# Performance work log

Hardware: AMD Instinct MI355X
Metric: run time of the kernel (lower is better)

## Reference

```python
import jax, jax.numpy as jnp
import numpy as np

# Hardcoded hyperparameters from the torch module
E = 128   # n_embd
H = 4     # n_head
HS = 32   # head_size = n_embd // n_head
L = 4     # n_layer
T = 512   # block_size (full context)
V = 512   # vocab_size (quantization_levels)
B = 64    # batch
SCALE = 0.02  # init std per _init_weights


def _ln(x, g, b):
    mu = x.mean(-1, keepdims=True)
    var = ((x - mu) ** 2).mean(-1, keepdims=True)
    return (x - mu) / jnp.sqrt(var + 1e-5) * g + b


def setup_inputs() -> dict:
    key = jax.random.key(0)
    ks = jax.random.split(key, 24)
    rn = lambda k, shape: SCALE * jax.random.normal(k, shape, dtype=jnp.float32)
    return {
        "idx": jax.random.randint(ks[0], (B, T), 0, V),
        "tok_emb": rn(ks[1], (V, E)),
        "pos_emb": rn(ks[2], (T, E)),
        # per-head projections, stacked over layers and heads: x[...,E] @ wq[l,h] -> [...,HS]
        "wq": rn(ks[3], (L, H, E, HS)),
        "wk": rn(ks[4], (L, H, E, HS)),
        "wv": rn(ks[5], (L, H, E, HS)),
        "w_proj": rn(ks[6], (L, E, E)),   # torch Linear weight layout [out, in]
        "b_proj": jnp.zeros((L, E), jnp.float32),
        "ln1_g": jnp.ones((L, E), jnp.float32),
        "ln1_b": jnp.zeros((L, E), jnp.float32),
        "ln2_g": jnp.ones((L, E), jnp.float32),
        "ln2_b": jnp.zeros((L, E), jnp.float32),
        "w1": rn(ks[7], (L, 4 * E, E)),
        "b1": jnp.zeros((L, 4 * E), jnp.float32),
        "w2": rn(ks[8], (L, E, 4 * E)),
        "b2": jnp.zeros((L, E), jnp.float32),
        "lnf_g": jnp.ones((E,), jnp.float32),
        "lnf_b": jnp.zeros((E,), jnp.float32),
        "w_head": rn(ks[9], (V, E)),
        "b_head": jnp.zeros((V,), jnp.float32),
    }


def reference(idx, tok_emb, pos_emb, wq, wk, wv, w_proj, b_proj,
              ln1_g, ln1_b, ln2_g, ln2_b, w1, b1, w2, b2,
              lnf_g, lnf_b, w_head, b_head):
    Bv, Tv = idx.shape
    x = tok_emb[idx] + pos_emb[None, :Tv, :]          # [B,T,E]
    causal = jnp.tril(jnp.ones((Tv, Tv), dtype=bool))
    for l in range(L):
        h = _ln(x, ln1_g[l], ln1_b[l])
        q = jnp.einsum('bte,hed->bhtd', h, wq[l])     # [B,H,T,HS]
        k = jnp.einsum('bte,hed->bhtd', h, wk[l])
        v = jnp.einsum('bte,hed->bhtd', h, wv[l])
        s = jnp.einsum('bhtd,bhsd->bhts', q, k) * (HS ** -0.5)
        s = jnp.where(causal, s, -jnp.inf)
        a = jax.nn.softmax(s, axis=-1)
        o = jnp.einsum('bhts,bhsd->bhtd', a, v)       # [B,H,T,HS]
        o = o.transpose(0, 2, 1, 3).reshape(Bv, Tv, E)  # concat heads
        x = x + o @ w_proj[l].T + b_proj[l]
        h = _ln(x, ln2_g[l], ln2_b[l])
        x = x + jax.nn.gelu(h @ w1[l].T + b1[l], approximate=False) @ w2[l].T + b2[l]
    x = _ln(x, lnf_g, lnf_b)
    logits = x @ w_head.T + b_head                    # [B,T,V]
    return logits
```

## Files before the change

kernel.cpp:

```cpp
#include <hip/hip_runtime.h>

typedef __bf16 bf16x8 __attribute__((ext_vector_type(8)));
typedef __bf16 bf16x2 __attribute__((ext_vector_type(2)));
typedef float f32x4 __attribute__((ext_vector_type(4)));

constexpr int E_ = 128, H_ = 4, HS_ = 32, L_ = 4, T_ = 512, V_ = 512, B_ = 64;
constexpr int M_ = B_ * T_;

__device__ __forceinline__ float b2f(ushort u) {
    return __uint_as_float(((uint)u) << 16);
}
__device__ __forceinline__ ushort f2b(float f) {
    uint x = __float_as_uint(f);
    uint r = (x + 0x7fffu + ((x >> 16) & 1u)) >> 16;
    return (ushort)r;
}
__device__ __forceinline__ uint packbf(float a, float b) {
    bf16x2 t; t[0] = (__bf16)a; t[1] = (__bf16)b;
    return __builtin_bit_cast(uint, t);
}

constexpr int kNSeg = 19;
constexpr int kOffs[kNSeg + 1] = {
    0, 65536, 131072, 196608, 262144, 327680, 393216, 393728, 394240, 394752,
    395264, 395776, 657920, 659968, 922112, 922624, 922752, 922880, 988416, 988928
};
constexpr int kTotal = 988928;

struct SrcPtrs { const void* p[kNSeg]; };

__global__ __launch_bounds__(256) void k_convert(SrcPtrs sp, ushort* __restrict__ arena) {
    int gid = blockIdx.x * 256 + threadIdx.x;
    if (gid >= kTotal) return;
    bool isf32 = (((const uint*)sp.p[7])[0] == 0x3F800000u);
    int s = 0;
    #pragma unroll
    for (int i = 1; i < kNSeg; i++) if (gid >= kOffs[i]) s = i;
    int local = gid - kOffs[s];
    ushort v;
    if (isf32) v = f2b(((const float*)sp.p[s])[local]);
    else       v = ((const ushort*)sp.p[s])[local];
    arena[gid] = v;
}

__global__ void k_prep_qkv(const ushort* __restrict__ wq, const ushort* __restrict__ wk,
                           const ushort* __restrict__ wv, ushort* __restrict__ wt) {
    int gid = blockIdx.x * 256 + threadIdx.x;
    if (gid >= L_ * 384 * E_) return;
    int e = gid & 127;
    int n = (gid >> 7) % 384;
    int l = gid / (384 * E_);
    int part = n >> 7, within = n & 127, hh = within >> 5, d = within & 31;
    const ushort* src = part == 0 ? wq : (part == 1 ? wk : wv);
    wt[gid] = src[(((size_t)(l * H_ + hh) * E_) + e) * HS_ + d];
}

__global__ __launch_bounds__(256) void k_embed_ln(const int* __restrict__ idx,
                                                  const ushort* __restrict__ tok,
                                                  const ushort* __restrict__ pos,
                                                  const ushort* __restrict__ g,
                                                  const ushort* __restrict__ beta,
                                                  float* __restrict__ x, ushort* __restrict__ h) {
    int wave = threadIdx.x >> 6, lane = threadIdx.x & 63;
    int row = blockIdx.x * 4 + wave;
    int t = row & (T_ - 1);
    int id = idx[row];
    float v0 = b2f(tok[id * E_ + lane])      + b2f(pos[t * E_ + lane]);
    float v1 = b2f(tok[id * E_ + lane + 64]) + b2f(pos[t * E_ + lane + 64]);
    size_t o = (size_t)row * E_;
    x[o + lane] = v0; x[o + lane + 64] = v1;
    float s = v0 + v1;
    #pragma unroll
    for (int m = 32; m; m >>= 1) s += __shfl_xor(s, m, 64);
    float mu = s * (1.0f / 128.0f);
    float d0 = v0 - mu, d1 = v1 - mu;
    float ss = d0 * d0 + d1 * d1;
    #pragma unroll
    for (int m = 32; m; m >>= 1) ss += __shfl_xor(ss, m, 64);
    float rstd = rsqrtf(ss * (1.0f / 128.0f) + 1e-5f);
    h[o + lane]      = f2b(d0 * rstd * b2f(g[lane])      + b2f(beta[lane]));
    h[o + lane + 64] = f2b(d1 * rstd * b2f(g[lane + 64]) + b2f(beta[lane + 64]));
}

template<int EPI>
__global__ __launch_bounds__(256) void k_gemm(const ushort* __restrict__ A, const ushort* __restrict__ W,
                                              const ushort* __restrict__ bias, void* __restrict__ outp,
                                              void* __restrict__ outp2,
                                              const ushort* __restrict__ lng, const ushort* __restrict__ lnb,
                                              const uint* __restrict__ dtraw, int K, int lda, int ldc) {
    int wid = threadIdx.x >> 6, lane = threadIdx.x & 63;
    int wr = wid >> 1, wc = wid & 1;
    int bm = blockIdx.x, bn = blockIdx.y;
    int r16 = lane & 15, kq = lane >> 4;
    const ushort* Abase = A + (size_t)(bm * 128 + wr * 64 + r16) * lda + kq * 8;
    const ushort* Wbase = W + (size_t)(bn * 128 + wc * 64 + r16) * K + kq * 8;
    bool f32out = false;
    if constexpr (EPI == 1) f32out = (dtraw[0] == 0x3F800000u);
    f32x4 acc[4][4];
    #pragma unroll
    for (int i = 0; i < 4; i++)
        #pragma unroll
        for (int j = 0; j < 4; j++) acc[i][j] = (f32x4)0.0f;
    for (int k0 = 0; k0 < K; k0 += 32) {
        bf16x8 af[4], wf[4];
        #pragma unroll
        for (int mi = 0; mi < 4; mi++)
            af[mi] = *(const bf16x8*)(Abase + (size_t)mi * 16 * lda + k0);
        #pragma unroll
        for (int ni = 0; ni < 4; ni++)
            wf[ni] = *(const bf16x8*)(Wbase + (size_t)ni * 16 * K + k0);
        #pragma unroll
        for (int mi = 0; mi < 4; mi++)
            #pragma unroll
            for (int ni = 0; ni < 4; ni++)
                acc[mi][ni] = __builtin_amdgcn_mfma_f32_16x16x32_bf16(af[mi], wf[ni], acc[mi][ni], 0, 0, 0);
    }
    int orow0 = bm * 128 + wr * 64 + kq * 4;
    int ocol0 = bn * 128 + wc * 64 + r16;
    if constexpr (EPI == 5) {
        __shared__ float lnS[2][128], lnQ[2][128];
        float*  xg = (float*)outp;
        ushort* hg = (ushort*)outp2;
        #pragma unroll
        for (int ni = 0; ni < 4; ni++) {
            int col = ocol0 + ni * 16;
            float bv = b2f(bias[col]);
            #pragma unroll
            for (int mi = 0; mi < 4; mi++) {
                #pragma unroll
                for (int e = 0; e < 4; e++) {
                    size_t gi = (size_t)(orow0 + mi * 16 + e) * 128 + col;
                    float xv = xg[gi] + acc[mi][ni][e] + bv;
                    xg[gi] = xv;
                    acc[mi][ni][e] = xv;
                }
            }
        }
        #pragma unroll
        for (int mi = 0; mi < 4; mi++) {
            #pragma unroll
            for (int e = 0; e < 4; e++) {
                float s = 0.f, q = 0.f;
                #pragma unroll
                for (int ni = 0; ni < 4; ni++) { float v = acc[mi][ni][e]; s += v; q += v * v; }
                #pragma unroll
                for (int mk = 1; mk < 16; mk <<= 1) {
                    s += __shfl_xor(s, mk, 64); q += __shfl_xor(q, mk, 64);
                }
                if (r16 == 0) {
                    int lrow = wr * 64 + mi * 16 + kq * 4 + e;
                    lnS[wc][lrow] = s; lnQ[wc][lrow] = q;
                }
            }
        }
        __syncthreads();
        float gc[4], bc[4];
        #pragma unroll
        for (int ni = 0; ni < 4; ni++) {
            int col = ocol0 + ni * 16;
            gc[ni] = b2f(lng[col]); bc[ni] = b2f(lnb[col]);
        }
        #pragma unroll
        for (int mi = 0; mi < 4; mi++) {
            #pragma unroll
            for (int e = 0; e < 4; e++) {
                int lrow = wr * 64 + mi * 16 + kq * 4 + e;
                float tot = lnS[0][lrow] + lnS[1][lrow];
                float tq  = lnQ[0][lrow] + lnQ[1][lrow];
                float mu  = tot * (1.0f / 128.0f);
                float var = tq * (1.0f / 128.0f) - mu * mu;
                float rstd = rsqrtf(var + 1e-5f);
                size_t grow = (size_t)(bm * 128 + lrow) * 128;
                #pragma unroll
                for (int ni = 0; ni < 4; ni++) {
                    int col = ocol0 + ni * 16;
                    hg[grow + col] = f2b((acc[mi][ni][e] - mu) * rstd * gc[ni] + bc[ni]);
                }
            }
        }
        return;
    }
    if constexpr (EPI == 4) {
        if (bn == 2) {
            ushort* vt = (ushort*)outp2;
            #pragma unroll
            for (int mi = 0; mi < 4; mi++) {
                int row0 = orow0 + mi * 16;
                int bb = row0 >> 9, tt = row0 & 511;
                #pragma unroll
                for (int ni = 0; ni < 4; ni++) {
                    int vd = (ocol0 - 256) + ni * 16;
                    int hh = vd >> 5, dd = vd & 31;
                    ushort4 pk;
                    pk.x = f2b(acc[mi][ni][0]); pk.y = f2b(acc[mi][ni][1]);
                    pk.z = f2b(acc[mi][ni][2]); pk.w = f2b(acc[mi][ni][3]);
                    *(ushort4*)(vt + (((size_t)(bb * 4 + hh) * 32 + dd) << 9) + tt) = pk;
                }
            }
            return;
        }
    }
    #pragma unroll
    for (int mi = 0; mi < 4; mi++) {
        #pragma unroll
        for (int ni = 0; ni < 4; ni++) {
            int col = ocol0 + ni * 16;
            float bv = 0.0f;
            if constexpr (EPI == 1 || EPI == 2) bv = b2f(bias[col]);
            #pragma unroll
            for (int e = 0; e < 4; e++) {
                int row = orow0 + mi * 16 + e;
                float v = acc[mi][ni][e] + bv;
                if constexpr (EPI == 2) v = 0.5f * v * (1.0f + erff(v * 0.70710678118f));
                if constexpr (EPI == 1) {
                    if (f32out) ((float*)outp)[(size_t)row * ldc + col] = v;
                    else        ((ushort*)outp)[(size_t)row * ldc + col] = f2b(v);
                } else {
                    ((ushort*)outp)[(size_t)row * ldc + col] = f2b(v);
                }
            }
        }
    }
}

constexpr float SC_ = 0.2550348637f;

__device__ __forceinline__ bf16x8 scale8(bf16x8 v, float s) {
    bf16x8 r;
    #pragma unroll
    for (int i = 0; i < 8; i++) r[i] = (__bf16)((float)v[i] * s);
    return r;
}

__device__ __forceinline__ bf16x8 relayoutP(const float* p, int r16, int g) {
    uint pk00 = packbf(p[0], p[1]), pk01 = packbf(p[2], p[3]);
    uint pk10 = packbf(p[4], p[5]), pk11 = packbf(p[6], p[7]);
    int ga = ((g & 1) << 5) + r16;
    int gb = ga + 16;
    uint A0 = (uint)__shfl((int)pk00, ga), A1 = (uint)__shfl((int)pk01, ga);
    uint C0 = (uint)__shfl((int)pk00, gb), C1 = (uint)__shfl((int)pk01, gb);
    uint B0 = (uint)__shfl((int)pk10, ga), B1 = (uint)__shfl((int)pk11, ga);
    uint D0 = (uint)__shfl((int)pk10, gb), D1 = (uint)__shfl((int)pk11, gb);
    bool hi2 = g >= 2;
    uint4 pr;
    pr.x = hi2 ? B0 : A0; pr.y = hi2 ? B1 : A1;
    pr.z = hi2 ? D0 : C0; pr.w = hi2 ? D1 : C1;
    return __builtin_bit_cast(bf16x8, pr);
}

__global__ __launch_bounds__(256) void k_attn_proj(const ushort* __restrict__ qk,
                                                   const ushort* __restrict__ vt,
                                                   const ushort* __restrict__ wproj,
                                                   const ushort* __restrict__ bproj,
                                                   const ushort* __restrict__ lng,
                                                   const ushort* __restrict__ lnb,
                                                   float* __restrict__ x,
                                                   ushort* __restrict__ h) {
    __shared__ ushort olds[32 * 128];
    __shared__ float lnS[4][32], lnQ[4][32];
    int lane = threadIdx.x & 63, w = threadIdx.x >> 6;
    int r16 = lane & 15, g = lane >> 4;
    int bid = blockIdx.x;
    int b = (bid & 7) * 8 + (bid >> 7);
    int p = (bid >> 3) & 15;
    int qbaseA = p * 16, qbaseB = (31 - p) * 16;
    int myqA = qbaseA + r16, myqB = qbaseB + r16;
    int qmaxA = qbaseA + 15, qmaxB = qbaseB + 15;
    const ushort* qkbase = qk + (size_t)b * 512 * 256;
    bf16x8 qfA = scale8(*(const bf16x8*)(qkbase + (size_t)(qbaseA + r16) * 256 + w * 32 + g * 8), SC_);
    bf16x8 qfB = scale8(*(const bf16x8*)(qkbase + (size_t)(qbaseB + r16) * 256 + w * 32 + g * 8), SC_);
    const ushort* kptr = qkbase + 128 + w * 32 + g * 8;
    const ushort* vbase = vt + ((size_t)(b * 4 + w) * 32) * 512;

    f32x4 oA0 = (f32x4)0.0f, oA1 = (f32x4)0.0f, oB0 = (f32x4)0.0f, oB1 = (f32x4)0.0f;
    float psA = 0.0f, psB = 0.0f;
    for (int j0 = 0; j0 <= qmaxB; j0 += 32) {
        bf16x8 kf0 = *(const bf16x8*)(kptr + (size_t)(j0 + r16) * 256);
        bf16x8 kf1 = *(const bf16x8*)(kptr + (size_t)(j0 + 16 + r16) * 256);
        bf16x8 vf0 = *(const bf16x8*)(vbase + (size_t)r16 * 512 + j0 + g * 8);
        bf16x8 vf1 = *(const bf16x8*)(vbase + (size_t)(16 + r16) * 512 + j0 + g * 8);
        {
            f32x4 s0 = __builtin_amdgcn_mfma_f32_16x16x32_bf16(kf0, qfB, (f32x4)0.0f, 0, 0, 0);
            f32x4 s1 = __builtin_amdgcn_mfma_f32_16x16x32_bf16(kf1, qfB, (f32x4)0.0f, 0, 0, 0);
            float pv[8];
            #pragma unroll
            for (int e = 0; e < 4; e++) {
                int ja = j0 + 4 * g + e;
                pv[e]     = (ja      <= myqB) ? exp2f(s0[e]) : 0.0f;
                pv[4 + e] = (ja + 16 <= myqB) ? exp2f(s1[e]) : 0.0f;
                psB += pv[e] + pv[4 + e];
            }
            bf16x8 pf = relayoutP(pv, r16, g);
            oB0 = __builtin_amdgcn_mfma_f32_16x16x32_bf16(vf0, pf, oB0, 0, 0, 0);
            oB1 = __builtin_amdgcn_mfma_f32_16x16x32_bf16(vf1, pf, oB1, 0, 0, 0);
        }
        if (j0 <= qmaxA) {
            f32x4 s0 = __builtin_amdgcn_mfma_f32_16x16x32_bf16(kf0, qfA, (f32x4)0.0f, 0, 0, 0);
            f32x4 s1 = __builtin_amdgcn_mfma_f32_16x16x32_bf16(kf1, qfA, (f32x4)0.0f, 0, 0, 0);
            float pv[8];
            #pragma unroll
            for (int e = 0; e < 4; e++) {
                int ja = j0 + 4 * g + e;
                pv[e]     = (ja      <= myqA) ? exp2f(s0[e]) : 0.0f;
                pv[4 + e] = (ja + 16 <= myqA) ? exp2f(s1[e]) : 0.0f;
                psA += pv[e] + pv[4 + e];
            }
            bf16x8 pf = relayoutP(pv, r16, g);
            oA0 = __builtin_amdgcn_mfma_f32_16x16x32_bf16(vf0, pf, oA0, 0, 0, 0);
            oA1 = __builtin_amdgcn_mfma_f32_16x16x32_bf16(vf1, pf, oA1, 0, 0, 0);
        }
    }
    psA += __shfl_xor(psA, 16, 64); psA += __shfl_xor(psA, 32, 64);
    psB += __shfl_xor(psB, 16, 64); psB += __shfl_xor(psB, 32, 64);
    {
        float invA = 1.0f / psA, invB = 1.0f / psB;
        int sw = (r16 & 7) << 4;
        int baseA = r16 * 256 + w * 64 + g * 8;
        int baseB = (16 + r16) * 256 + w * 64 + g * 8;
        uint2 a0, a1, b0, b1;
        a0.x = packbf(oA0[0] * invA, oA0[1] * invA); a0.y = packbf(oA0[2] * invA, oA0[3] * invA);
        a1.x = packbf(oA1[0] * invA, oA1[1] * invA); a1.y = packbf(oA1[2] * invA, oA1[3] * invA);
        b0.x = packbf(oB0[0] * invB, oB0[1] * invB); b0.y = packbf(oB0[2] * invB, oB0[3] * invB);
        b1.x = packbf(oB1[0] * invB, oB1[1] * invB); b1.y = packbf(oB1[2] * invB, oB1[3] * invB);
        *(uint2*)((char*)olds + (baseA ^ sw))        = a0;
        *(uint2*)((char*)olds + ((baseA + 32) ^ sw)) = a1;
        *(uint2*)((char*)olds + (baseB ^ sw))        = b0;
        *(uint2*)((char*)olds + ((baseB + 32) ^ sw)) = b1;
    }
    __syncthreads();
    f32x4 acc[2][2];
    acc[0][0] = (f32x4)0.0f; acc[0][1] = (f32x4)0.0f;
    acc[1][0] = (f32x4)0.0f; acc[1][1] = (f32x4)0.0f;
    const ushort* wp0 = wproj + (size_t)(w * 32 + r16) * 128 + g * 8;
    const ushort* wp1 = wp0 + (size_t)16 * 128;
    #pragma unroll
    for (int kk = 0; kk < 4; kk++) {
        bf16x8 w0 = *(const bf16x8*)(wp0 + kk * 32);
        bf16x8 w1 = *(const bf16x8*)(wp1 + kk * 32);
        #pragma unroll
        for (int mi = 0; mi < 2; mi++) {
            int abyte = ((mi * 16 + r16) * 256 + kk * 64 + g * 16) ^ ((r16 & 7) << 4);
            bf16x8 af = *(const bf16x8*)((const char*)olds + abyte);
            acc[mi][0] = __builtin_amdgcn_mfma_f32_16x16x32_bf16(af, w0, acc[mi][0], 0, 0, 0);
            acc[mi][1] = __builtin_amdgcn_mfma_f32_16x16x32_bf16(af, w1, acc[mi][1], 0, 0, 0);
        }
    }
    int col0 = w * 32 + r16, col1 = col0 + 16;
    float bv0 = b2f(bproj[col0]), bv1 = b2f(bproj[col1]);
    float xv[2][2][4];
    #pragma unroll
    for (int mi = 0; mi < 2; mi++) {
        int qb = mi == 0 ? qbaseA : qbaseB;
        #pragma unroll
        for (int e = 0; e < 4; e++) {
            size_t gi = (size_t)(b * 512 + qb + g * 4 + e) * 128;
            float v0 = x[gi + col0] + acc[mi][0][e] + bv0;
            float v1 = x[gi + col1] + acc[mi][1][e] + bv1;
            x[gi + col0] = v0; x[gi + col1] = v1;
            xv[mi][0][e] = v0; xv[mi][1][e] = v1;
        }
    }
    #pragma unroll
    for (int mi = 0; mi < 2; mi++) {
        #pragma unroll
        for (int e = 0; e < 4; e++) {
            float s = xv[mi][0][e] + xv[mi][1][e];
            float q = xv[mi][0][e] * xv[mi][0][e] + xv[mi][1][e] * xv[mi][1][e];
            #pragma unroll
            for (int mk = 1; mk < 16; mk <<= 1) {
                s += __shfl_xor(s, mk, 64); q += __shfl_xor(q, mk, 64);
            }
            if (r16 == 0) { lnS[w][mi * 16 + g * 4 + e] = s; lnQ[w][mi * 16 + g * 4 + e] = q; }
        }
    }
    __syncthreads();
    float g0 = b2f(lng[col0]), g1 = b2f(lng[col1]);
    float be0 = b2f(lnb[col0]), be1 = b2f(lnb[col1]);
    #pragma unroll
    for (int mi = 0; mi < 2; mi++) {
        int qb = mi == 0 ? qbaseA : qbaseB;
        #pragma unroll
        for (int e = 0; e < 4; e++) {
            int lr = mi * 16 + g * 4 + e;
            float tot = lnS[0][lr] + lnS[1][lr] + lnS[2][lr] + lnS[3][lr];
            float tq  = lnQ[0][lr] + lnQ[1][lr] + lnQ[2][lr] + lnQ[3][lr];
            float mu  = tot * (1.0f / 128.0f);
            float var = tq * (1.0f / 128.0f) - mu * mu;
            float rstd = rsqrtf(var + 1e-5f);
            size_t gr = (size_t)(b * 512 + qb + g * 4 + e) * 128;
            h[gr + col0] = f2b((xv[mi][0][e] - mu) * rstd * g0 + be0);
            h[gr + col1] = f2b((xv[mi][1][e] - mu) * rstd * g1 + be1);
        }
    }
}

extern "C" void kernel_launch(void* const* d_in, const int* in_sizes, int n_in,
                              void* d_out, int out_size, void* d_ws, size_t ws_size,
                              hipStream_t stream) {
    const int* idx = (const int*)d_in[0];

    char* ws = (char*)d_ws;
    float*  x     = (float*) (ws + 0);
    ushort* h     = (ushort*)(ws + (16u << 20));
    ushort* wqkvt = (ushort*)(ws + (24u << 20));
    ushort* arena = (ushort*)(ws + (25u << 20));

    ushort* qkv = (ushort*)d_out;
    ushort* vt  = (ushort*)d_out + (12u << 20);
    ushort* mid = (ushort*)d_out;

    const ushort* tok    = arena + kOffs[0];
    const ushort* pos    = arena + kOffs[1];
    const ushort* wqp    = arena + kOffs[2];
    const ushort* wkp    = arena + kOffs[3];
    const ushort* wvp    = arena + kOffs[4];
    const ushort* w_proj = arena + kOffs[5];
    const ushort* b_proj = arena + kOffs[6];
    const ushort* ln1_g  = arena + kOffs[7];
    const ushort* ln1_b  = arena + kOffs[8];
    const ushort* ln2_g  = arena + kOffs[9];
    const ushort* ln2_b  = arena + kOffs[10];
    const ushort* w1     = arena + kOffs[11];
    const ushort* b1     = arena + kOffs[12];
    const ushort* w2     = arena + kOffs[13];
    const ushort* b2     = arena + kOffs[14];
    const ushort* lnf_g  = arena + kOffs[15];
    const ushort* lnf_b  = arena + kOffs[16];
    const ushort* w_head = arena + kOffs[17];
    const ushort* b_head = arena + kOffs[18];

    SrcPtrs sp;
    for (int i = 0; i < kNSeg; i++) sp.p[i] = d_in[i + 1];
    k_convert<<<(kTotal + 255) / 256, 256, 0, stream>>>(sp, arena);

    k_prep_qkv<<<768, 256, 0, stream>>>(wqp, wkp, wvp, wqkvt);
    k_embed_ln<<<M_ / 4, 256, 0, stream>>>(idx, tok, pos, ln1_g, ln1_b, x, h);
    for (int l = 0; l < L_; l++) {
        const ushort* ng = (l < 3) ? (ln1_g + (l + 1) * E_) : lnf_g;
        const ushort* nb = (l < 3) ? (ln1_b + (l + 1) * E_) : lnf_b;
        k_gemm<4><<<dim3(M_ / 128, 3), 256, 0, stream>>>(h, wqkvt + (size_t)l * 384 * E_, nullptr,
                                                         qkv, vt, nullptr, nullptr, nullptr, 128, 128, 256);
        k_attn_proj<<<1024, 256, 0, stream>>>(qkv, vt, w_proj + (size_t)l * E_ * E_, b_proj + l * E_,
                                              ln2_g + l * E_, ln2_b + l * E_, x, h);
        k_gemm<2><<<dim3(M_ / 128, 4), 256, 0, stream>>>(h, w1 + (size_t)l * 4 * E_ * E_, b1 + l * 4 * E_,
                                                         mid, nullptr, nullptr, nullptr, nullptr, 128, 128, 512);
        k_gemm<5><<<dim3(M_ / 128, 1), 256, 0, stream>>>(mid, w2 + (size_t)l * E_ * 4 * E_, b2 + l * E_,
                                                         x, h, ng, nb, nullptr, 512, 512, 128);
    }
    k_gemm<1><<<dim3(M_ / 128, 4), 256, 0, stream>>>(h, w_head, b_head, d_out, nullptr,
                                                     nullptr, nullptr, (const uint*)d_in[8], 128, 128, 512);
}
```

Baseline: 500.3 us.

## Fuse MLP up/down GEMMs into one kernel with LDS-resident hidden activations

Replaces the separate W1+GELU GEMM and the W2+residual+LayerNorm GEMM with a single kernel. Each 64-row block computes the 512-wide hidden layer in four 128-column chunks, keeps each GELU'd chunk in swizzled LDS, and accumulates the down projection in registers. This avoids writing and re-reading the large bf16 intermediate in global memory and removes one launch per layer. The attention loop also gains register double-buffering of K/V loads. The cost is extra syncthreads per chunk and more register pressure.

Result: faster. 457.2 us (-8.6%).

```diff
diff --git a/kernel.cpp b/kernel.cpp
--- a/kernel.cpp
+++ b/kernel.cpp
@@ -86,7 +86,6 @@
 __global__ __launch_bounds__(256) void k_gemm(const ushort* __restrict__ A, const ushort* __restrict__ W,
                                               const ushort* __restrict__ bias, void* __restrict__ outp,
                                               void* __restrict__ outp2,
-                                              const ushort* __restrict__ lng, const ushort* __restrict__ lnb,
                                               const uint* __restrict__ dtraw, int K, int lda, int ldc) {
     int wid = threadIdx.x >> 6, lane = threadIdx.x & 63;
     int wr = wid >> 1, wc = wid & 1;
@@ -117,69 +116,6 @@
     }
     int orow0 = bm * 128 + wr * 64 + kq * 4;
     int ocol0 = bn * 128 + wc * 64 + r16;
-    if constexpr (EPI == 5) {
-        __shared__ float lnS[2][128], lnQ[2][128];
-        float*  xg = (float*)outp;
-        ushort* hg = (ushort*)outp2;
-        #pragma unroll
-        for (int ni = 0; ni < 4; ni++) {
-            int col = ocol0 + ni * 16;
-            float bv = b2f(bias[col]);
-            #pragma unroll
-            for (int mi = 0; mi < 4; mi++) {
-                #pragma unroll
-                for (int e = 0; e < 4; e++) {
-                    size_t gi = (size_t)(orow0 + mi * 16 + e) * 128 + col;
-                    float xv = xg[gi] + acc[mi][ni][e] + bv;
-                    xg[gi] = xv;
-                    acc[mi][ni][e] = xv;
-                }
-            }
-        }
-        #pragma unroll
-        for (int mi = 0; mi < 4; mi++) {
-            #pragma unroll
-            for (int e = 0; e < 4; e++) {
-                float s = 0.f, q = 0.f;
-                #pragma unroll
-                for (int ni = 0; ni < 4; ni++) { float v = acc[mi][ni][e]; s += v; q += v * v; }
-                #pragma unroll
-                for (int mk = 1; mk < 16; mk <<= 1) {
-                    s += __shfl_xor(s, mk, 64); q += __shfl_xor(q, mk, 64);
-                }
-                if (r16 == 0) {
-                    int lrow = wr * 64 + mi * 16 + kq * 4 + e;
-                    lnS[wc][lrow] = s; lnQ[wc][lrow] = q;
-                }
-            }
-        }
-        __syncthreads();
-        float gc[4], bc[4];
-        #pragma unroll
-        for (int ni = 0; ni < 4; ni++) {
-            int col = ocol0 + ni * 16;
-            gc[ni] = b2f(lng[col]); bc[ni] = b2f(lnb[col]);
-        }
-        #pragma unroll
-        for (int mi = 0; mi < 4; mi++) {
-            #pragma unroll
-            for (int e = 0; e < 4; e++) {
-                int lrow = wr * 64 + mi * 16 + kq * 4 + e;
-                float tot = lnS[0][lrow] + lnS[1][lrow];
-                float tq  = lnQ[0][lrow] + lnQ[1][lrow];
-                float mu  = tot * (1.0f / 128.0f);
-                float var = tq * (1.0f / 128.0f) - mu * mu;
-                float rstd = rsqrtf(var + 1e-5f);
-                size_t grow = (size_t)(bm * 128 + lrow) * 128;
-                #pragma unroll
-                for (int ni = 0; ni < 4; ni++) {
-                    int col = ocol0 + ni * 16;
-                    hg[grow + col] = f2b((acc[mi][ni][e] - mu) * rstd * gc[ni] + bc[ni]);
-                }
-            }
-        }
-        return;
-    }
     if constexpr (EPI == 4) {
         if (bn == 2) {
             ushort* vt = (ushort*)outp2;
@@ -206,12 +142,11 @@
         for (int ni = 0; ni < 4; ni++) {
             int col = ocol0 + ni * 16;
             float bv = 0.0f;
-            if constexpr (EPI == 1 || EPI == 2) bv = b2f(bias[col]);
+            if constexpr (EPI == 1) bv = b2f(bias[col]);
             #pragma unroll
             for (int e = 0; e < 4; e++) {
                 int row = orow0 + mi * 16 + e;
                 float v = acc[mi][ni][e] + bv;
-                if constexpr (EPI == 2) v = 0.5f * v * (1.0f + erff(v * 0.70710678118f));
                 if constexpr (EPI == 1) {
                     if (f32out) ((float*)outp)[(size_t)row * ldc + col] = v;
                     else        ((ushort*)outp)[(size_t)row * ldc + col] = f2b(v);
@@ -274,11 +209,19 @@
 
     f32x4 oA0 = (f32x4)0.0f, oA1 = (f32x4)0.0f, oB0 = (f32x4)0.0f, oB1 = (f32x4)0.0f;
     float psA = 0.0f, psB = 0.0f;
+    bf16x8 kf0 = *(const bf16x8*)(kptr + (size_t)r16 * 256);
+    bf16x8 kf1 = *(const bf16x8*)(kptr + (size_t)(16 + r16) * 256);
+    bf16x8 vf0 = *(const bf16x8*)(vbase + (size_t)r16 * 512 + g * 8);
+    bf16x8 vf1 = *(const bf16x8*)(vbase + (size_t)(16 + r16) * 512 + g * 8);
     for (int j0 = 0; j0 <= qmaxB; j0 += 32) {
-        bf16x8 kf0 = *(const bf16x8*)(kptr + (size_t)(j0 + r16) * 256);
-        bf16x8 kf1 = *(const bf16x8*)(kptr + (size_t)(j0 + 16 + r16) * 256);
-        bf16x8 vf0 = *(const bf16x8*)(vbase + (size_t)r16 * 512 + j0 + g * 8);
-        bf16x8 vf1 = *(const bf16x8*)(vbase + (size_t)(16 + r16) * 512 + j0 + g * 8);
+        int jn = j0 + 32;
+        bf16x8 nk0 = kf0, nk1 = kf1, nv0 = vf0, nv1 = vf1;
+        if (jn <= qmaxB) {
+            nk0 = *(const bf16x8*)(kptr + (size_t)(jn + r16) * 256);
+            nk1 = *(const bf16x8*)(kptr + (size_t)(jn + 16 + r16) * 256);
+            nv0 = *(const bf16x8*)(vbase + (size_t)r16 * 512 + jn + g * 8);
+            nv1 = *(const bf16x8*)(vbase + (size_t)(16 + r16) * 512 + jn + g * 8);
+        }
         {
             f32x4 s0 = __builtin_amdgcn_mfma_f32_16x16x32_bf16(kf0, qfB, (f32x4)0.0f, 0, 0, 0);
             f32x4 s1 = __builtin_amdgcn_mfma_f32_16x16x32_bf16(kf1, qfB, (f32x4)0.0f, 0, 0, 0);
@@ -309,6 +252,7 @@
             oA0 = __builtin_amdgcn_mfma_f32_16x16x32_bf16(vf0, pf, oA0, 0, 0, 0);
             oA1 = __builtin_amdgcn_mfma_f32_16x16x32_bf16(vf1, pf, oA1, 0, 0, 0);
         }
+        kf0 = nk0; kf1 = nk1; vf0 = nv0; vf1 = nv1;
     }
     psA += __shfl_xor(psA, 16, 64); psA += __shfl_xor(psA, 32, 64);
     psB += __shfl_xor(psB, 16, 64); psB += __shfl_xor(psB, 32, 64);
@@ -394,6 +338,120 @@
     }
 }
 
+__global__ __launch_bounds__(256) void k_mlp(ushort* __restrict__ h,
+                                             const ushort* __restrict__ w1,
+                                             const ushort* __restrict__ b1,
+                                             const ushort* __restrict__ w2,
+                                             const ushort* __restrict__ b2,
+                                             const ushort* __restrict__ lng,
+                                             const ushort* __restrict__ lnb,
+                                             float* __restrict__ x) {
+    __shared__ ushort mid[64 * 128];
+    __shared__ float lnS[4][64], lnQ[4][64];
+    int lane = threadIdx.x & 63, w = threadIdx.x >> 6;
+    int r16 = lane & 15, kq = lane >> 4;
+    int r0 = blockIdx.x * 64;
+    f32x4 acc2[4][2];
+    #pragma unroll
+    for (int mi = 0; mi < 4; mi++) { acc2[mi][0] = (f32x4)0.0f; acc2[mi][1] = (f32x4)0.0f; }
+    const ushort* Ab = h + (size_t)(r0 + r16) * 128 + kq * 8;
+    for (int c = 0; c < 4; c++) {
+        f32x4 acc1[4][2];
+        #pragma unroll
+        for (int mi = 0; mi < 4; mi++) { acc1[mi][0] = (f32x4)0.0f; acc1[mi][1] = (f32x4)0.0f; }
+        const ushort* W1b = w1 + (size_t)(c * 128 + w * 32 + r16) * 128 + kq * 8;
+        #pragma unroll
+        for (int kk = 0; kk < 4; kk++) {
+            bf16x8 wf0 = *(const bf16x8*)(W1b + kk * 32);
+            bf16x8 wf1 = *(const bf16x8*)(W1b + (size_t)16 * 128 + kk * 32);
+            #pragma unroll
+            for (int mi = 0; mi < 4; mi++) {
+                bf16x8 af = *(const bf16x8*)(Ab + (size_t)mi * 16 * 128 + kk * 32);
+                acc1[mi][0] = __builtin_amdgcn_mfma_f32_16x16x32_bf16(af, wf0, acc1[mi][0], 0, 0, 0);
+                acc1[mi][1] = __builtin_amdgcn_mfma_f32_16x16x32_bf16(af, wf1, acc1[mi][1], 0, 0, 0);
+            }
+        }
+        float bv0 = b2f(b1[c * 128 + w * 32 + r16]);
+        float bv1 = b2f(b1[c * 128 + w * 32 + 16 + r16]);
+        #pragma unroll
+        for (int mi = 0; mi < 4; mi++) {
+            #pragma unroll
+            for (int e = 0; e < 4; e++) {
+                int row = mi * 16 + kq * 4 + e;
+                int sw = (row & 7) << 4;
+                float v0 = acc1[mi][0][e] + bv0;
+                float v1 = acc1[mi][1][e] + bv1;
+                v0 = 0.5f * v0 * (1.0f + erff(v0 * 0.70710678118f));
+                v1 = 0.5f * v1 * (1.0f + erff(v1 * 0.70710678118f));
+                int c0 = (row * 256 + (w * 32 + r16) * 2) ^ sw;
+                int c1 = (row * 256 + (w * 32 + 16 + r16) * 2) ^ sw;
+                *(ushort*)((char*)mid + c0) = f2b(v0);
+                *(ushort*)((char*)mid + c1) = f2b(v1);
+            }
+        }
+        __syncthreads();
+        const ushort* W2b = w2 + (size_t)(w * 32 + r16) * 512 + c * 128 + kq * 8;
+        #pragma unroll
+        for (int kk = 0; kk < 4; kk++) {
+            bf16x8 wf0 = *(const bf16x8*)(W2b + kk * 32);
+            bf16x8 wf1 = *(const bf16x8*)(W2b + (size_t)16 * 512 + kk * 32);
+            #pragma unroll
+            for (int mi = 0; mi < 4; mi++) {
+                int abyte = ((mi * 16 + r16) * 256 + kk * 64 + kq * 16) ^ ((r16 & 7) << 4);
+                bf16x8 af = *(const bf16x8*)((const char*)mid + abyte);
+                acc2[mi][0] = __builtin_amdgcn_mfma_f32_16x16x32_bf16(af, wf0, acc2[mi][0], 0, 0, 0);
+                acc2[mi][1] = __builtin_amdgcn_mfma_f32_16x16x32_bf16(af, wf1, acc2[mi][1], 0, 0, 0);
+            }
+        }
+        __syncthreads();
+    }
+    int col0 = w * 32 + r16, col1 = col0 + 16;
+    float bv0 = b2f(b2[col0]), bv1 = b2f(b2[col1]);
+    float xv[4][2][4];
+    #pragma unroll
+    for (int mi = 0; mi < 4; mi++) {
+        #pragma unroll
+        for (int e = 0; e < 4; e++) {
+            size_t gi = (size_t)(r0 + mi * 16 + kq * 4 + e) * 128;
+            float v0 = x[gi + col0] + acc2[mi][0][e] + bv0;
+            float v1 = x[gi + col1] + acc2[mi][1][e] + bv1;
+            x[gi + col0] = v0; x[gi + col1] = v1;
+            xv[mi][0][e] = v0; xv[mi][1][e] = v1;
+        }
+    }
+    #pragma unroll
+    for (int mi = 0; mi < 4; mi++) {
+        #pragma unroll
+        for (int e = 0; e < 4; e++) {
+            float s = xv[mi][0][e] + xv[mi][1][e];
+            float q = xv[mi][0][e] * xv[mi][0][e] + xv[mi][1][e] * xv[mi][1][e];
+            #pragma unroll
+            for (int mk = 1; mk < 16; mk <<= 1) {
+                s += __shfl_xor(s, mk, 64); q += __shfl_xor(q, mk, 64);
+            }
+            if (r16 == 0) { lnS[w][mi * 16 + kq * 4 + e] = s; lnQ[w][mi * 16 + kq * 4 + e] = q; }
+        }
+    }
+    __syncthreads();
+    float g0 = b2f(lng[col0]), g1 = b2f(lng[col1]);
+    float be0 = b2f(lnb[col0]), be1 = b2f(lnb[col1]);
+    #pragma unroll
+    for (int mi = 0; mi < 4; mi++) {
+        #pragma unroll
+        for (int e = 0; e < 4; e++) {
+            int lr = mi * 16 + kq * 4 + e;
+            float tot = lnS[0][lr] + lnS[1][lr] + lnS[2][lr] + lnS[3][lr];
+            float tq  = lnQ[0][lr] + lnQ[1][lr] + lnQ[2][lr] + lnQ[3][lr];
+            float mu  = tot * (1.0f / 128.0f);
+            float var = tq * (1.0f / 128.0f) - mu * mu;
+            float rstd = rsqrtf(var + 1e-5f);
+            size_t gr = (size_t)(r0 + lr) * 128;
+            h[gr + col0] = f2b((xv[mi][0][e] - mu) * rstd * g0 + be0);
+            h[gr + col1] = f2b((xv[mi][1][e] - mu) * rstd * g1 + be1);
+        }
+    }
+}
+
 extern "C" void kernel_launch(void* const* d_in, const int* in_sizes, int n_in,
                               void* d_out, int out_size, void* d_ws, size_t ws_size,
                               hipStream_t stream) {
@@ -407,7 +465,6 @@
 
     ushort* qkv = (ushort*)d_out;
     ushort* vt  = (ushort*)d_out + (12u << 20);
-    ushort* mid = (ushort*)d_out;
 
     const ushort* tok    = arena + kOffs[0];
     const ushort* pos    = arena + kOffs[1];
@@ -439,14 +496,12 @@
         const ushort* ng = (l < 3) ? (ln1_g + (l + 1) * E_) : lnf_g;
         const ushort* nb = (l < 3) ? (ln1_b + (l + 1) * E_) : lnf_b;
         k_gemm<4><<<dim3(M_ / 128, 3), 256, 0, stream>>>(h, wqkvt + (size_t)l * 384 * E_, nullptr,
-                                                         qkv, vt, nullptr, nullptr, nullptr, 128, 128, 256);
+                                                         qkv, vt, nullptr, 128, 128, 256);
         k_attn_proj<<<1024, 256, 0, stream>>>(qkv, vt, w_proj + (size_t)l * E_ * E_, b_proj + l * E_,
                                               ln2_g + l * E_, ln2_b + l * E_, x, h);
-        k_gemm<2><<<dim3(M_ / 128, 4), 256, 0, stream>>>(h, w1 + (size_t)l * 4 * E_ * E_, b1 + l * 4 * E_,
-                                                         mid, nullptr, nullptr, nullptr, nullptr, 128, 128, 512);
-        k_gemm<5><<<dim3(M_ / 128, 1), 256, 0, stream>>>(mid, w2 + (size_t)l * E_ * 4 * E_, b2 + l * E_,
-                                                         x, h, ng, nb, nullptr, 512, 512, 128);
+        k_mlp<<<M_ / 64, 256, 0, stream>>>(h, w1 + (size_t)l * 4 * E_ * E_, b1 + l * 4 * E_,
+                                           w2 + (size_t)l * E_ * 4 * E_, b2 + l * E_, ng, nb, x);
     }
     k_gemm<1><<<dim3(M_ / 128, 4), 256, 0, stream>>>(h, w_head, b_head, d_out, nullptr,
-                                                     nullptr, nullptr, (const uint*)d_in[8], 128, 128, 512);
-}
+                                                     (const uint*)d_in[8], 128, 128, 512);
+}
```
